# Kernel optimization log

Hardware: AMD Instinct MI355X
Metric: run time of the kernel (lower is better)

Reference implementation:

```python
import jax, jax.numpy as jnp
import numpy as np

NUM_BINS = 40
EPS = 1e-8


def build_zg():
    # z_bin_ctrs[i] = i * pi/2 / 39, zg[i,j] = clamp(cos(|z_i - z_j|), 0, 1)
    z = jnp.arange(NUM_BINS, dtype=jnp.float32) * (np.pi / 2.0 / (NUM_BINS - 1))
    zg = jnp.cos(jnp.abs(z[:, None] - z[None, :]))
    return jnp.clip(zg, 0.0, 1.0)


def setup_inputs() -> dict:
    key = jax.random.key(0)
    k1, k2 = jax.random.split(key)
    batch_label = jax.random.randint(k1, (8192,), 0, NUM_BINS, dtype=jnp.int64 if jax.config.jax_enable_x64 else jnp.int32)
    batch_feat = jax.random.normal(k2, (8192, 512), dtype=jnp.float32)
    return {"batch_label": batch_label, "batch_feat": batch_feat}


def reference(batch_label, batch_feat):
    zg = build_zg()  # [40, 40] constant graph
    # label adjacency: zg gathered at (label_i, label_j) -> [bs, bs]
    lbl_adj = zg[batch_label[:, None], batch_label[None, :]]
    # feature adjacency: cosine-similarity Gram matrix
    # torch cosine_similarity uses denom = max(||x||*||y||, eps)
    norms = jnp.maximum(jnp.linalg.norm(batch_feat, axis=-1, keepdims=True), EPS)
    fn = batch_feat / norms
    feat_adj = fn @ fn.T  # [bs, bs]
    # MSE loss (mean over all bs*bs entries)
    diff = feat_adj - lbl_adj
    return jnp.mean(diff * diff)
```

## Files before the change

kernel.cpp:

```cpp
#include <hip/hip_runtime.h>
#include <hip/hip_bf16.h>


typedef __attribute__((ext_vector_type(8))) short bf16x8;
typedef __attribute__((ext_vector_type(4))) float f32x4;

#define NROW 8192
#define DIM  512
#define NBIN 40
#define NBLK 64
#define NPAIR (NBLK*(NBLK+1)/2)

__device__ __forceinline__ unsigned short f2bf(float x) {
  __hip_bfloat16 h = __float2bfloat16(x);
  union { __hip_bfloat16 h; unsigned short u; } cv;
  cv.h = h;
  return cv.u;
}

__global__ __launch_bounds__(256) void rownorm_kernel(const float* __restrict__ feat,
                                                      __hip_bfloat16* __restrict__ fn) {
  int wid  = threadIdx.x >> 6;
  int lane = threadIdx.x & 63;
  int row  = blockIdx.x * 4 + wid;
  const float4* src = (const float4*)(feat + (size_t)row * DIM);
  float4 a = src[lane];
  float4 b = src[lane + 64];
  float s = a.x*a.x + a.y*a.y + a.z*a.z + a.w*a.w
          + b.x*b.x + b.y*b.y + b.z*b.z + b.w*b.w;
#pragma unroll
  for (int off = 1; off < 64; off <<= 1) s += __shfl_xor(s, off, 64);
  float scale = 1.0f / fmaxf(sqrtf(s), 1e-8f);
  ushort4 o0, o1;
  o0.x = f2bf(a.x * scale); o0.y = f2bf(a.y * scale);
  o0.z = f2bf(a.z * scale); o0.w = f2bf(a.w * scale);
  o1.x = f2bf(b.x * scale); o1.y = f2bf(b.y * scale);
  o1.z = f2bf(b.z * scale); o1.w = f2bf(b.w * scale);
  ushort4* dst = (ushort4*)(fn + (size_t)row * DIM);
  dst[lane]      = o0;
  dst[lane + 64] = o1;
}

__global__ __launch_bounds__(256) void loss_kernel(const __hip_bfloat16* __restrict__ fn,
                                                   const int* __restrict__ label,
                                                   double* __restrict__ partials) {
  __shared__ __hip_bfloat16 As[128 * 32];
  __shared__ __hip_bfloat16 Bs[128 * 32];
  __shared__ float zg[NBIN * NBIN];
  __shared__ int   lbl[256];
  __shared__ float wsum[4];

  const int tid  = threadIdx.x;
  const int wid  = tid >> 6;
  const int lane = tid & 63;

  int t = blockIdx.x;
  int bi = 0;
  while (bi < NBLK - 1 && (bi + 1) * NBLK - ((bi + 1) * bi) / 2 <= t) bi++;
  int bj = bi + (t - (bi * NBLK - (bi * (bi - 1)) / 2));
  const int i0 = bi * 128;
  const int j0 = bj * 128;

  for (int idx = tid; idx < NBIN * NBIN; idx += 256) {
    int a = idx / NBIN, b = idx - a * NBIN;
    float d = fabsf((float)(a - b)) * (float)(1.5707963267948966 / (NBIN - 1));
    float c = cosf(d);
    zg[idx] = fminf(fmaxf(c, 0.0f), 1.0f);
  }
  if (tid < 128) lbl[tid] = label[i0 + tid];
  else           lbl[tid] = label[j0 + (tid - 128)];

  const int wr = wid >> 1;
  const int wc = wid & 1;

  f32x4 acc[4][4] = {};

  for (int kt = 0; kt < 16; ++kt) {
    const int k0 = kt * 32;
#pragma unroll
    for (int q = 0; q < 2; ++q) {
      const int L   = q * 256 + wid * 64 + lane;
      const int row = L >> 2;
      const int col = (L & 3) * 8;
      const int dstOff = (q * 256 + wid * 64) * 16;
      const __hip_bfloat16* gA = fn + (size_t)(i0 + row) * DIM + k0 + col;
      const __hip_bfloat16* gB = fn + (size_t)(j0 + row) * DIM + k0 + col;
      __builtin_amdgcn_global_load_lds(
          (const __attribute__((address_space(1))) void*)gA,
          (__attribute__((address_space(3))) void*)((char*)As + dstOff), 16, 0, 0);
      __builtin_amdgcn_global_load_lds(
          (const __attribute__((address_space(1))) void*)gB,
          (__attribute__((address_space(3))) void*)((char*)Bs + dstOff), 16, 0, 0);
    }
    __syncthreads();

    bf16x8 af[4], bfr[4];
#pragma unroll
    for (int m = 0; m < 4; ++m)
      af[m] = *(const bf16x8*)&As[(wr * 64 + m * 16 + (lane & 15)) * 32 + (lane >> 4) * 8];
#pragma unroll
    for (int n = 0; n < 4; ++n)
      bfr[n] = *(const bf16x8*)&Bs[(wc * 64 + n * 16 + (lane & 15)) * 32 + (lane >> 4) * 8];
#pragma unroll
    for (int m = 0; m < 4; ++m)
#pragma unroll
      for (int n = 0; n < 4; ++n)
        acc[m][n] = __builtin_amdgcn_mfma_f32_16x16x32_bf16(af[m], bfr[n], acc[m][n], 0, 0, 0);
    __syncthreads();
  }

  const int ccol  = lane & 15;
  const int rbase = (lane >> 4) * 4;
  float lsum = 0.0f;
#pragma unroll
  for (int n = 0; n < 4; ++n) {
    const int lj = lbl[128 + wc * 64 + n * 16 + ccol];
#pragma unroll
    for (int m = 0; m < 4; ++m) {
#pragma unroll
      for (int r = 0; r < 4; ++r) {
        const int li = lbl[wr * 64 + m * 16 + rbase + r];
        float d = acc[m][n][r] - zg[li * NBIN + lj];
        lsum += d * d;
      }
    }
  }
  if (bi != bj) lsum *= 2.0f;

#pragma unroll
  for (int off = 1; off < 64; off <<= 1) lsum += __shfl_xor(lsum, off, 64);
  if (lane == 0) wsum[wid] = lsum;
  __syncthreads();
  if (tid == 0)
    partials[blockIdx.x] = (double)((wsum[0] + wsum[1]) + (wsum[2] + wsum[3]));
}

__global__ __launch_bounds__(256) void finalize_kernel(const double* __restrict__ partials,
                                                       int nblk, float* __restrict__ out) {
  __shared__ double wsh[4];
  int wid = threadIdx.x >> 6, lane = threadIdx.x & 63;
  double s = 0.0;
  for (int i = threadIdx.x; i < nblk; i += 256) s += partials[i];
#pragma unroll
  for (int off = 1; off < 64; off <<= 1) s += __shfl_xor(s, off, 64);
  if (lane == 0) wsh[wid] = s;
  __syncthreads();
  if (threadIdx.x == 0) {
    double tot = wsh[0] + wsh[1] + wsh[2] + wsh[3];
    out[0] = (float)(tot / ((double)NROW * (double)NROW));
  }
}

extern "C" void kernel_launch(void* const* d_in, const int* in_sizes, int n_in,
                              void* d_out, int out_size, void* d_ws, size_t ws_size,
                              hipStream_t stream) {
  const int*   label = (const int*)d_in[0];
  const float* feat  = (const float*)d_in[1];
  float* out = (float*)d_out;

  char* ws = (char*)d_ws;
  __hip_bfloat16* fn = (__hip_bfloat16*)ws;
  double* partials = (double*)(ws + (size_t)NROW * DIM * 2);

  rownorm_kernel<<<NROW / 4, 256, 0, stream>>>(feat, fn);
  loss_kernel<<<NPAIR, 256, 0, stream>>>(fn, label, partials);
  finalize_kernel<<<1, 256, 0, stream>>>(partials, NPAIR, out);
}
```

Baseline: 122.8 us.

## Use 256x256 tiles with triple-buffered async LDS pipeline and swizzled layout

Doubles the symmetric Gram tile to 256x256 with 512-thread blocks (8 waves, each 128x64). Global-to-LDS loads are issued two k-steps ahead into a three-stage ring buffer, interleaved with MFMA phases and fine-grained barriers and setprio. An XOR swizzle on LDS column groups reduces bank conflicts, and block indices are remapped across XCDs. This is meant to raise data reuse and hide load latency, at the cost of fewer blocks (528) and higher register and LDS pressure.

New measurement: 122.1 us. Within noise of the previous version (-0.6%).

```diff
diff --git a/kernel.cpp b/kernel.cpp
--- a/kernel.cpp
+++ b/kernel.cpp
@@ -8,8 +8,11 @@
 #define NROW 8192
 #define DIM  512
 #define NBIN 40
-#define NBLK 64
+#define NBLK 32
 #define NPAIR (NBLK*(NBLK+1)/2)
+#define BK 32
+#define NT (DIM/BK)
+#define TELEM (256*BK)
 
 __device__ __forceinline__ unsigned short f2bf(float x) {
   __hip_bfloat16 h = __float2bfloat16(x);
@@ -41,86 +44,138 @@
   dst[lane + 64] = o1;
 }
 
-__global__ __launch_bounds__(256) void loss_kernel(const __hip_bfloat16* __restrict__ fn,
-                                                   const int* __restrict__ label,
-                                                   double* __restrict__ partials) {
-  __shared__ __hip_bfloat16 As[128 * 32];
-  __shared__ __hip_bfloat16 Bs[128 * 32];
+__global__ __launch_bounds__(512, 2) void loss_kernel(const __hip_bfloat16* __restrict__ fn,
+                                                      const int* __restrict__ label,
+                                                      double* __restrict__ partials) {
+  __shared__ __hip_bfloat16 Abuf[3][TELEM];
+  __shared__ __hip_bfloat16 Bbuf[3][TELEM];
   __shared__ float zg[NBIN * NBIN];
-  __shared__ int   lbl[256];
-  __shared__ float wsum[4];
+  __shared__ int   lbl[512];
+  __shared__ float wsum[8];
 
   const int tid  = threadIdx.x;
   const int wid  = tid >> 6;
   const int lane = tid & 63;
-
-  int t = blockIdx.x;
+  const int wm   = wid >> 2;
+  const int wn   = wid & 3;
+
+  const int t0 = (blockIdx.x & 7) * (NPAIR / 8) + (blockIdx.x >> 3);
+
   int bi = 0;
-  while (bi < NBLK - 1 && (bi + 1) * NBLK - ((bi + 1) * bi) / 2 <= t) bi++;
-  int bj = bi + (t - (bi * NBLK - (bi * (bi - 1)) / 2));
-  const int i0 = bi * 128;
-  const int j0 = bj * 128;
-
-  for (int idx = tid; idx < NBIN * NBIN; idx += 256) {
+  while (bi < NBLK - 1 && (bi + 1) * NBLK - ((bi + 1) * bi) / 2 <= t0) bi++;
+  const int bj = bi + (t0 - (bi * NBLK - (bi * (bi - 1)) / 2));
+  const int i0 = bi * 256;
+  const int j0 = bj * 256;
+
+  for (int idx = tid; idx < NBIN * NBIN; idx += 512) {
     int a = idx / NBIN, b = idx - a * NBIN;
     float d = fabsf((float)(a - b)) * (float)(1.5707963267948966 / (NBIN - 1));
-    float c = cosf(d);
-    zg[idx] = fminf(fmaxf(c, 0.0f), 1.0f);
-  }
-  if (tid < 128) lbl[tid] = label[i0 + tid];
-  else           lbl[tid] = label[j0 + (tid - 128)];
-
-  const int wr = wid >> 1;
-  const int wc = wid & 1;
-
-  f32x4 acc[4][4] = {};
-
-  for (int kt = 0; kt < 16; ++kt) {
-    const int k0 = kt * 32;
-#pragma unroll
-    for (int q = 0; q < 2; ++q) {
-      const int L   = q * 256 + wid * 64 + lane;
-      const int row = L >> 2;
-      const int col = (L & 3) * 8;
-      const int dstOff = (q * 256 + wid * 64) * 16;
-      const __hip_bfloat16* gA = fn + (size_t)(i0 + row) * DIM + k0 + col;
-      const __hip_bfloat16* gB = fn + (size_t)(j0 + row) * DIM + k0 + col;
+    zg[idx] = fminf(fmaxf(cosf(d), 0.0f), 1.0f);
+  }
+  lbl[tid] = (tid < 256) ? label[i0 + tid] : label[j0 + tid - 256];
+
+  const __hip_bfloat16* srcA[2];
+  const __hip_bfloat16* srcB[2];
+  int dstOff[2];
+#pragma unroll
+  for (int q = 0; q < 2; ++q) {
+    const int L   = tid + q * 512;
+    const int row = L >> 2;
+    const int cg  = (L & 3) ^ ((row >> 1) & 3);
+    srcA[q] = fn + (size_t)(i0 + row) * DIM + cg * 8;
+    srcB[q] = fn + (size_t)(j0 + row) * DIM + cg * 8;
+    dstOff[q] = (q * 512 + wid * 64) * 16;
+  }
+
+  auto issueA = [&](int tt, int bb) {
+#pragma unroll
+    for (int q = 0; q < 2; ++q)
       __builtin_amdgcn_global_load_lds(
-          (const __attribute__((address_space(1))) void*)gA,
-          (__attribute__((address_space(3))) void*)((char*)As + dstOff), 16, 0, 0);
+          (const __attribute__((address_space(1))) void*)(srcA[q] + tt * BK),
+          (__attribute__((address_space(3))) void*)((char*)&Abuf[bb][0] + dstOff[q]),
+          16, 0, 0);
+  };
+  auto issueB = [&](int tt, int bb) {
+#pragma unroll
+    for (int q = 0; q < 2; ++q)
       __builtin_amdgcn_global_load_lds(
-          (const __attribute__((address_space(1))) void*)gB,
-          (__attribute__((address_space(3))) void*)((char*)Bs + dstOff), 16, 0, 0);
-    }
-    __syncthreads();
-
-    bf16x8 af[4], bfr[4];
-#pragma unroll
-    for (int m = 0; m < 4; ++m)
-      af[m] = *(const bf16x8*)&As[(wr * 64 + m * 16 + (lane & 15)) * 32 + (lane >> 4) * 8];
-#pragma unroll
-    for (int n = 0; n < 4; ++n)
-      bfr[n] = *(const bf16x8*)&Bs[(wc * 64 + n * 16 + (lane & 15)) * 32 + (lane >> 4) * 8];
-#pragma unroll
-    for (int m = 0; m < 4; ++m)
-#pragma unroll
-      for (int n = 0; n < 4; ++n)
-        acc[m][n] = __builtin_amdgcn_mfma_f32_16x16x32_bf16(af[m], bfr[n], acc[m][n], 0, 0, 0);
-    __syncthreads();
-  }
-
-  const int ccol  = lane & 15;
-  const int rbase = (lane >> 4) * 4;
+          (const __attribute__((address_space(1))) void*)(srcB[q] + tt * BK),
+          (__attribute__((address_space(3))) void*)((char*)&Bbuf[bb][0] + dstOff[q]),
+          16, 0, 0);
+  };
+
+  issueA(0, 0); issueB(0, 0);
+  issueA(1, 1); issueB(1, 1);
+  asm volatile("s_waitcnt vmcnt(4)" ::: "memory");
+  __builtin_amdgcn_s_barrier();
+
+  f32x4 acc[8][4] = {};
+  const int fr = lane & 15;
+  const int fc = lane >> 4;
+  const int cx = fc ^ ((fr >> 1) & 3);
+  const int arow0 = wm * 128 + fr;
+  const int brow0 = wn * 64 + fr;
+
+  int rb = 0;
+  for (int t = 0; t < NT; ++t) {
+    const __hip_bfloat16* Ab = &Abuf[rb][0];
+    const __hip_bfloat16* Bb = &Bbuf[rb][0];
+    const int pb = (rb >= 1) ? rb - 1 : rb + 2;
+
+    bf16x8 a0[4], bv[4];
+#pragma unroll
+    for (int mf = 0; mf < 4; ++mf)
+      a0[mf] = *(const bf16x8*)&Ab[(arow0 + mf * 16) * BK + cx * 8];
+#pragma unroll
+    for (int nf = 0; nf < 4; ++nf)
+      bv[nf] = *(const bf16x8*)&Bb[(brow0 + nf * 16) * BK + cx * 8];
+    if (t < NT - 2) issueA(t + 2, pb);
+    __builtin_amdgcn_s_barrier();
+    asm volatile("s_waitcnt lgkmcnt(0)" ::: "memory");
+    __builtin_amdgcn_s_setprio(1);
+#pragma unroll
+    for (int mf = 0; mf < 4; ++mf)
+#pragma unroll
+      for (int nf = 0; nf < 4; ++nf)
+        acc[mf][nf] = __builtin_amdgcn_mfma_f32_16x16x32_bf16(a0[mf], bv[nf], acc[mf][nf], 0, 0, 0);
+    __builtin_amdgcn_s_setprio(0);
+    __builtin_amdgcn_s_barrier();
+
+    bf16x8 a1[4];
+#pragma unroll
+    for (int mf = 0; mf < 4; ++mf)
+      a1[mf] = *(const bf16x8*)&Ab[(arow0 + 64 + mf * 16) * BK + cx * 8];
+    if (t < NT - 2) issueB(t + 2, pb);
+    __builtin_amdgcn_s_barrier();
+    asm volatile("s_waitcnt lgkmcnt(0)" ::: "memory");
+    __builtin_amdgcn_s_setprio(1);
+#pragma unroll
+    for (int mf = 0; mf < 4; ++mf)
+#pragma unroll
+      for (int nf = 0; nf < 4; ++nf)
+        acc[4 + mf][nf] = __builtin_amdgcn_mfma_f32_16x16x32_bf16(a1[mf], bv[nf], acc[4 + mf][nf], 0, 0, 0);
+    __builtin_amdgcn_s_setprio(0);
+
+    if (t < NT - 2)       asm volatile("s_waitcnt vmcnt(4)" ::: "memory");
+    else if (t == NT - 2) asm volatile("s_waitcnt vmcnt(0)" ::: "memory");
+    __builtin_amdgcn_s_barrier();
+    rb = (rb + 1 >= 3) ? 0 : rb + 1;
+  }
+
+  const int rb4 = (lane >> 4) * 4;
+  int ljv[4];
+#pragma unroll
+  for (int nf = 0; nf < 4; ++nf) ljv[nf] = lbl[256 + wn * 64 + nf * 16 + fr];
   float lsum = 0.0f;
 #pragma unroll
-  for (int n = 0; n < 4; ++n) {
-    const int lj = lbl[128 + wc * 64 + n * 16 + ccol];
-#pragma unroll
-    for (int m = 0; m < 4; ++m) {
-#pragma unroll
-      for (int r = 0; r < 4; ++r) {
-        const int li = lbl[wr * 64 + m * 16 + rbase + r];
-        float d = acc[m][n][r] - zg[li * NBIN + lj];
+  for (int mf = 0; mf < 8; ++mf) {
+#pragma unroll
+    for (int r = 0; r < 4; ++r) {
+      const int li = lbl[wm * 128 + mf * 16 + rb4 + r];
+      const float* zrow = &zg[li * NBIN];
+#pragma unroll
+      for (int nf = 0; nf < 4; ++nf) {
+        float d = acc[mf][nf][r] - zrow[ljv[nf]];
         lsum += d * d;
       }
     }
@@ -131,8 +186,12 @@
   for (int off = 1; off < 64; off <<= 1) lsum += __shfl_xor(lsum, off, 64);
   if (lane == 0) wsum[wid] = lsum;
   __syncthreads();
-  if (tid == 0)
-    partials[blockIdx.x] = (double)((wsum[0] + wsum[1]) + (wsum[2] + wsum[3]));
+  if (tid == 0) {
+    double s = 0.0;
+#pragma unroll
+    for (int w = 0; w < 8; ++w) s += (double)wsum[w];
+    partials[blockIdx.x] = s;
+  }
 }
 
 __global__ __launch_bounds__(256) void finalize_kernel(const double* __restrict__ partials,
@@ -163,6 +222,6 @@
   double* partials = (double*)(ws + (size_t)NROW * DIM * 2);
 
   rownorm_kernel<<<NROW / 4, 256, 0, stream>>>(feat, fn);
-  loss_kernel<<<NPAIR, 256, 0, stream>>>(fn, label, partials);
+  loss_kernel<<<NPAIR, 512, 0, stream>>>(fn, label, partials);
   finalize_kernel<<<1, 256, 0, stream>>>(partials, NPAIR, out);
 }
```

## Double-buffer LDS tiles with swizzle, XCD-aware block remap, and 1D zg lookup

Applied to the files above, without the earlier changes.

Restructures the GEMM-loss kernel so the next K tile is prefetched into a second LDS buffer while MFMAs run on the current one, leaving one barrier per step instead of two. It XOR-swizzles the LDS column groups to cut bank conflicts, remaps block IDs so each XCD gets a contiguous range of tile pairs, and replaces the 40x40 zg table with a 40-entry table indexed by |li-lj|. It also adds s_setprio around the MFMAs and an occupancy hint in launch_bounds. The cost is double the LDS per block and hand-written waitcnt ordering that must stay correct.

Result: faster. 116.0 us (-5.5%).

```diff
diff --git a/kernel.cpp b/kernel.cpp
--- a/kernel.cpp
+++ b/kernel.cpp
@@ -10,6 +10,9 @@
 #define NBIN 40
 #define NBLK 64
 #define NPAIR (NBLK*(NBLK+1)/2)
+#define BK 32
+#define NT (DIM/BK)
+#define TELEM (128*BK)
 
 __device__ __forceinline__ unsigned short f2bf(float x) {
   __hip_bfloat16 h = __float2bfloat16(x);
@@ -41,86 +44,118 @@
   dst[lane + 64] = o1;
 }
 
-__global__ __launch_bounds__(256) void loss_kernel(const __hip_bfloat16* __restrict__ fn,
-                                                   const int* __restrict__ label,
-                                                   double* __restrict__ partials) {
-  __shared__ __hip_bfloat16 As[128 * 32];
-  __shared__ __hip_bfloat16 Bs[128 * 32];
-  __shared__ float zg[NBIN * NBIN];
+__global__ __launch_bounds__(256, 4) void loss_kernel(const __hip_bfloat16* __restrict__ fn,
+                                                      const int* __restrict__ label,
+                                                      double* __restrict__ partials) {
+  __shared__ __hip_bfloat16 Abuf[2][TELEM];
+  __shared__ __hip_bfloat16 Bbuf[2][TELEM];
+  __shared__ float zd[NBIN];
   __shared__ int   lbl[256];
   __shared__ float wsum[4];
 
   const int tid  = threadIdx.x;
   const int wid  = tid >> 6;
   const int lane = tid & 63;
-
-  int t = blockIdx.x;
+  const int wr   = wid >> 1;
+  const int wc   = wid & 1;
+
+  const int t0 = (blockIdx.x & 7) * (NPAIR / 8) + (blockIdx.x >> 3);
+
   int bi = 0;
-  while (bi < NBLK - 1 && (bi + 1) * NBLK - ((bi + 1) * bi) / 2 <= t) bi++;
-  int bj = bi + (t - (bi * NBLK - (bi * (bi - 1)) / 2));
+  while (bi < NBLK - 1 && (bi + 1) * NBLK - ((bi + 1) * bi) / 2 <= t0) bi++;
+  const int bj = bi + (t0 - (bi * NBLK - (bi * (bi - 1)) / 2));
   const int i0 = bi * 128;
   const int j0 = bj * 128;
 
-  for (int idx = tid; idx < NBIN * NBIN; idx += 256) {
-    int a = idx / NBIN, b = idx - a * NBIN;
-    float d = fabsf((float)(a - b)) * (float)(1.5707963267948966 / (NBIN - 1));
-    float c = cosf(d);
-    zg[idx] = fminf(fmaxf(c, 0.0f), 1.0f);
-  }
-  if (tid < 128) lbl[tid] = label[i0 + tid];
-  else           lbl[tid] = label[j0 + (tid - 128)];
-
-  const int wr = wid >> 1;
-  const int wc = wid & 1;
+  if (tid < NBIN) {
+    float d = (float)tid * (float)(1.5707963267948966 / (NBIN - 1));
+    zd[tid] = fminf(fmaxf(cosf(d), 0.0f), 1.0f);
+  }
+  lbl[tid] = (tid < 128) ? label[i0 + tid] : label[j0 + tid - 128];
+
+  const __hip_bfloat16* srcA[2];
+  const __hip_bfloat16* srcB[2];
+  int dstOff[2];
+#pragma unroll
+  for (int q = 0; q < 2; ++q) {
+    const int L   = q * 256 + tid;
+    const int row = L >> 2;
+    const int cg  = (L & 3) ^ ((row >> 1) & 3);
+    srcA[q] = fn + (size_t)(i0 + row) * DIM + cg * 8;
+    srcB[q] = fn + (size_t)(j0 + row) * DIM + cg * 8;
+    dstOff[q] = (q * 256 + wid * 64) * 16;
+  }
+
+  auto issueTile = [&](int tt, int bb) {
+#pragma unroll
+    for (int q = 0; q < 2; ++q)
+      __builtin_amdgcn_global_load_lds(
+          (const __attribute__((address_space(1))) void*)(srcA[q] + tt * BK),
+          (__attribute__((address_space(3))) void*)((char*)&Abuf[bb][0] + dstOff[q]),
+          16, 0, 0);
+#pragma unroll
+    for (int q = 0; q < 2; ++q)
+      __builtin_amdgcn_global_load_lds(
+          (const __attribute__((address_space(1))) void*)(srcB[q] + tt * BK),
+          (__attribute__((address_space(3))) void*)((char*)&Bbuf[bb][0] + dstOff[q]),
+          16, 0, 0);
+  };
+
+  issueTile(0, 0);
+  asm volatile("s_waitcnt vmcnt(0)" ::: "memory");
+  __builtin_amdgcn_s_barrier();
 
   f32x4 acc[4][4] = {};
-
-  for (int kt = 0; kt < 16; ++kt) {
-    const int k0 = kt * 32;
-#pragma unroll
-    for (int q = 0; q < 2; ++q) {
-      const int L   = q * 256 + wid * 64 + lane;
-      const int row = L >> 2;
-      const int col = (L & 3) * 8;
-      const int dstOff = (q * 256 + wid * 64) * 16;
-      const __hip_bfloat16* gA = fn + (size_t)(i0 + row) * DIM + k0 + col;
-      const __hip_bfloat16* gB = fn + (size_t)(j0 + row) * DIM + k0 + col;
-      __builtin_amdgcn_global_load_lds(
-          (const __attribute__((address_space(1))) void*)gA,
-          (__attribute__((address_space(3))) void*)((char*)As + dstOff), 16, 0, 0);
-      __builtin_amdgcn_global_load_lds(
-          (const __attribute__((address_space(1))) void*)gB,
-          (__attribute__((address_space(3))) void*)((char*)Bs + dstOff), 16, 0, 0);
+  const int fr = lane & 15;
+  const int fc = lane >> 4;
+  const int cx = fc ^ ((fr >> 1) & 3);
+  const int arow0 = wr * 64 + fr;
+  const int brow0 = wc * 64 + fr;
+
+  for (int t = 0; t < NT; ++t) {
+    const int c = t & 1;
+    const __hip_bfloat16* Ab = &Abuf[c][0];
+    const __hip_bfloat16* Bb = &Bbuf[c][0];
+
+    bf16x8 af[4], bf[4];
+#pragma unroll
+    for (int m = 0; m < 4; ++m)
+      af[m] = *(const bf16x8*)&Ab[(arow0 + m * 16) * BK + cx * 8];
+#pragma unroll
+    for (int n = 0; n < 4; ++n)
+      bf[n] = *(const bf16x8*)&Bb[(brow0 + n * 16) * BK + cx * 8];
+
+    if (t < NT - 1) issueTile(t + 1, c ^ 1);
+
+    asm volatile("s_waitcnt lgkmcnt(0)" ::: "memory");
+    __builtin_amdgcn_s_setprio(1);
+#pragma unroll
+    for (int m = 0; m < 4; ++m)
+#pragma unroll
+      for (int n = 0; n < 4; ++n)
+        acc[m][n] = __builtin_amdgcn_mfma_f32_16x16x32_bf16(af[m], bf[n], acc[m][n], 0, 0, 0);
+    __builtin_amdgcn_s_setprio(0);
+
+    if (t < NT - 1) {
+      asm volatile("s_waitcnt vmcnt(0)" ::: "memory");
+      __builtin_amdgcn_s_barrier();
     }
-    __syncthreads();
-
-    bf16x8 af[4], bfr[4];
-#pragma unroll
-    for (int m = 0; m < 4; ++m)
-      af[m] = *(const bf16x8*)&As[(wr * 64 + m * 16 + (lane & 15)) * 32 + (lane >> 4) * 8];
-#pragma unroll
-    for (int n = 0; n < 4; ++n)
-      bfr[n] = *(const bf16x8*)&Bs[(wc * 64 + n * 16 + (lane & 15)) * 32 + (lane >> 4) * 8];
-#pragma unroll
-    for (int m = 0; m < 4; ++m)
-#pragma unroll
-      for (int n = 0; n < 4; ++n)
-        acc[m][n] = __builtin_amdgcn_mfma_f32_16x16x32_bf16(af[m], bfr[n], acc[m][n], 0, 0, 0);
-    __syncthreads();
-  }
-
-  const int ccol  = lane & 15;
-  const int rbase = (lane >> 4) * 4;
+  }
+
+  const int rb4 = (lane >> 4) * 4;
+  int ljv[4];
+#pragma unroll
+  for (int n = 0; n < 4; ++n) ljv[n] = lbl[128 + wc * 64 + n * 16 + fr];
   float lsum = 0.0f;
 #pragma unroll
-  for (int n = 0; n < 4; ++n) {
-    const int lj = lbl[128 + wc * 64 + n * 16 + ccol];
-#pragma unroll
-    for (int m = 0; m < 4; ++m) {
-#pragma unroll
-      for (int r = 0; r < 4; ++r) {
-        const int li = lbl[wr * 64 + m * 16 + rbase + r];
-        float d = acc[m][n][r] - zg[li * NBIN + lj];
+  for (int m = 0; m < 4; ++m) {
+#pragma unroll
+    for (int r = 0; r < 4; ++r) {
+      const int li = lbl[wr * 64 + m * 16 + rb4 + r];
+#pragma unroll
+      for (int n = 0; n < 4; ++n) {
+        int dd = li - ljv[n]; if (dd < 0) dd = -dd;
+        float d = acc[m][n][r] - zd[dd];
         lsum += d * d;
       }
     }
```
